# Optimization experiments

Hardware: AMD Instinct MI355X
Metric: run time of the kernel (lower is better)

The kernel has to match this reference:

```python
import jax, jax.numpy as jnp
import numpy as np

N_NODES = 100000
N_FEATS = 512
HIDDEN = 64
NUM_SAMPLES = 5
NUM_CLASSES = 16
BATCH = 16384


def setup_inputs() -> dict:
    key = jax.random.key(0)
    k1, k2, k3, k4, k5, k6, k7 = jax.random.split(key, 7)
    nodes = jax.random.randint(k1, (BATCH,), 0, N_NODES, dtype=jnp.int64) if jax.config.jax_enable_x64 else jax.random.randint(k1, (BATCH,), 0, N_NODES, dtype=jnp.int32)
    neigh_idx = jax.random.randint(k2, (N_NODES, NUM_SAMPLES), 0, N_NODES, dtype=jnp.int32)
    features = jax.random.normal(k3, (N_NODES, N_FEATS), dtype=jnp.float32)
    # xavier-uniform style init
    def xavier(k, shape):
        fan_in, fan_out = shape[1], shape[0]
        lim = jnp.sqrt(6.0 / (fan_in + fan_out)).astype(jnp.float32)
        return jax.random.uniform(k, shape, jnp.float32, -lim, lim)
    w1 = xavier(k4, (HIDDEN, 2 * N_FEATS))      # enc1 weight
    w2 = xavier(k5, (HIDDEN, 2 * HIDDEN))       # enc2 weight
    w_cls = xavier(k6, (NUM_CLASSES, HIDDEN))   # classifier weight
    return {"features": features, "w1": w1, "w2": w2, "w_cls": w_cls,
            "nodes": nodes, "neigh_idx": neigh_idx}


def reference(features, w1, w2, w_cls, nodes, neigh_idx):
    # Layer 1 (enc1, gcn=False): concat(self, mean(sampled neighbors)) -> W1 -> ReLU
    # Computed for all nodes (superset of what torch computes lazily; same values).
    neigh1 = features[neigh_idx].mean(axis=1)                      # [N, F]
    h1 = jax.nn.relu(jnp.concatenate([features, neigh1], axis=1) @ w1.T)  # [N, H]
    # Layer 2 (enc2) on the query batch
    self2 = h1[nodes]                                              # [B, H]
    neigh2 = h1[neigh_idx[nodes]].mean(axis=1)                     # [B, H]
    h2 = jax.nn.relu(jnp.concatenate([self2, neigh2], axis=1) @ w2.T)     # [B, H]
    # scores = (w_cls @ h2.T).T == h2 @ w_cls.T
    return h2 @ w_cls.T                                            # [B, C]
```

## Files before the change

kernel.cpp:

```cpp
#include <hip/hip_runtime.h>
#include <hip/hip_bf16.h>

#define N_NODES 100000
#define N_FEATS 512
#define HIDDEN 64
#define NUM_SAMPLES 5
#define NUM_CLASSES 16
#define BATCH 16384
#define N_TILES (N_NODES / 16)

typedef __attribute__((ext_vector_type(8))) short bf16x8;
typedef __attribute__((ext_vector_type(8))) unsigned short u16x8;
typedef __attribute__((ext_vector_type(4))) float f32x4;

static __device__ __forceinline__ float bf2f(unsigned short s) {
    unsigned int u = ((unsigned int)s) << 16;
    return __builtin_bit_cast(float, u);
}
static __device__ __forceinline__ short f2bf(float v) {
    __hip_bfloat16 b = __float2bfloat16(v);
    return *reinterpret_cast<short*>(&b);
}
static __device__ __forceinline__ int clampi(int v) {
    return ((unsigned)v < (unsigned)N_NODES) ? v : 0;
}

__global__ __launch_bounds__(256) void prep(const float* __restrict__ w1f,
                                            short* __restrict__ w1p,
                                            const int* __restrict__ nodes_i32,
                                            int* __restrict__ flag) {
    const int t = blockIdx.x * 256 + threadIdx.x;
    if (t < 64 * 1024) {
        const int j = t & 7;
        const int lane = (t >> 3) & 63;
        const int nb = (t >> 9) & 7;
        const int kk = t >> 12;
        const int l16 = lane & 15, quad = lane >> 4;
        const int cn = nb * 16 + l16;
        const int h = cn & 63, part = cn >> 6;
        w1p[t] = f2bf(w1f[h * 1024 + part * 512 + kk * 32 + quad * 8 + j]);
    }
    if (blockIdx.x == 0 && threadIdx.x == 0) {
        int odd_nonzero = 0;
        for (int i = 0; i < 64; i++)
            if (nodes_i32[2 * i + 1] != 0) odd_nonzero++;
        *flag = (odd_nonzero == 0) ? 1 : 0;
    }
}

__global__ __launch_bounds__(512) void pq_gemm(const float* __restrict__ feat,
                                               const short* __restrict__ w1p,
                                               short* __restrict__ PQ) {
    __shared__ __align__(16) short at[16 * 512];
    const int wave = threadIdx.x >> 6;
    const int lane = threadIdx.x & 63;
    const int quad = lane >> 4;
    const int l16  = lane & 15;
    const int tidr = threadIdx.x >> 5;
    const int tids = threadIdx.x & 31;

    bf16x8 bfrag[16];
#pragma unroll
    for (int kk = 0; kk < 16; kk++)
        bfrag[kk] = *reinterpret_cast<const bf16x8*>(
            w1p + (size_t)kk * 4096 + wave * 512 + lane * 8);

    const int stride = gridDim.x;
    f32x4 ra[2][2];

#define LOAD_TILE(tt)                                                             \
    {                                                                             \
        const float* base = feat + (size_t)((tt) * 16 + tidr) * N_FEATS + tids * 8;\
        _Pragma("unroll")                                                         \
        for (int i = 0; i < 2; i++) {                                             \
            ra[i][0] = *reinterpret_cast<const f32x4*>(base + i * 256);           \
            ra[i][1] = *reinterpret_cast<const f32x4*>(base + i * 256 + 4);       \
        }                                                                         \
    }

    int t = blockIdx.x;
    if (t < N_TILES) LOAD_TILE(t)

    for (; t < N_TILES; t += stride) {
        __syncthreads();
#pragma unroll
        for (int i = 0; i < 2; i++) {
            bf16x8 p;
#pragma unroll
            for (int j = 0; j < 4; j++) {
                p[j]     = f2bf(ra[i][0][j]);
                p[4 + j] = f2bf(ra[i][1][j]);
            }
            const int chunk = i * 32 + tids;
            const int cs = chunk ^ (tidr & 7);
            *reinterpret_cast<bf16x8*>(at + tidr * 512 + cs * 8) = p;
        }
        const int tn = t + stride;
        if (tn < N_TILES) LOAD_TILE(tn)
        __syncthreads();

        f32x4 acc = (f32x4){0.f, 0.f, 0.f, 0.f};
#pragma unroll
        for (int kk = 0; kk < 16; kk++) {
            const int chunk = kk * 4 + quad;
            const int cs = chunk ^ (l16 & 7);
            bf16x8 afrag = *reinterpret_cast<const bf16x8*>(at + l16 * 512 + cs * 8);
            acc = __builtin_amdgcn_mfma_f32_16x16x32_bf16(afrag, bfrag[kk], acc, 0, 0, 0);
        }

        const int cn = wave * 16 + l16;
#pragma unroll
        for (int r = 0; r < 4; r++) {
            const int row = t * 16 + quad * 4 + r;
            PQ[(size_t)row * 128 + cn] = f2bf(acc[r]);
        }
    }
#undef LOAD_TILE
}

__global__ __launch_bounds__(256) void h1_combine(const short* __restrict__ PQ,
                                                  const int* __restrict__ neigh_idx,
                                                  short* __restrict__ H1) {
    const int t = blockIdx.x * 256 + threadIdx.x;
    const int n = t >> 3;
    const int sub = t & 7;
    if (n >= N_NODES) return;

    u16x8 pv = *reinterpret_cast<const u16x8*>(PQ + (size_t)n * 128 + sub * 8);
    float s[8];
#pragma unroll
    for (int j = 0; j < 8; j++) s[j] = 0.f;
#pragma unroll
    for (int i = 0; i < NUM_SAMPLES; i++) {
        const int ni = clampi(neigh_idx[n * NUM_SAMPLES + i]);
        u16x8 qv = *reinterpret_cast<const u16x8*>(PQ + (size_t)ni * 128 + 64 + sub * 8);
#pragma unroll
        for (int j = 0; j < 8; j++) s[j] += bf2f(qv[j]);
    }
    u16x8 ov;
#pragma unroll
    for (int j = 0; j < 8; j++) {
        float v = bf2f(pv[j]) + 0.2f * s[j];
        v = v > 0.f ? v : 0.f;
        ov[j] = (unsigned short)f2bf(v);
    }
    *reinterpret_cast<u16x8*>(H1 + (size_t)n * 64 + sub * 8) = ov;
}

__global__ __launch_bounds__(256) void layer2_cls(const short* __restrict__ H1,
                                                  const int* __restrict__ nodes_i32,
                                                  const int* __restrict__ neigh_idx,
                                                  const float* __restrict__ w2,
                                                  const float* __restrict__ wcls,
                                                  const int* __restrict__ flag,
                                                  float* __restrict__ out) {
    __shared__ float gbuf[16][128];
    __shared__ float h2buf[16][64];
    const int wave = threadIdx.x >> 6;
    const int lane = threadIdx.x & 63;
    const int is64 = *flag;
    const int b0 = blockIdx.x * 16;

#pragma unroll
    for (int it = 0; it < 4; it++) {
        const int item = wave * 4 + it;
        const int b = b0 + item;
        const int node = clampi(nodes_i32[is64 ? 2 * b : b]);
        float selfv = bf2f((unsigned short)H1[(size_t)node * 64 + lane]);
        float ns = 0.f;
#pragma unroll
        for (int s = 0; s < NUM_SAMPLES; s++) {
            const int ni = clampi(neigh_idx[node * NUM_SAMPLES + s]);
            ns += bf2f((unsigned short)H1[(size_t)ni * 64 + lane]);
        }
        gbuf[item][lane] = selfv;
        gbuf[item][64 + lane] = 0.2f * ns;
    }
    __syncthreads();

    float acc[4] = {0.f, 0.f, 0.f, 0.f};
    const f32x4* w2r = reinterpret_cast<const f32x4*>(w2 + lane * 128);
#pragma unroll 8
    for (int k = 0; k < 32; k++) {
        f32x4 w = w2r[k];
#pragma unroll
        for (int it = 0; it < 4; it++) {
            f32x4 g = *reinterpret_cast<const f32x4*>(&gbuf[wave * 4 + it][k * 4]);
            acc[it] += g[0] * w[0] + g[1] * w[1] + g[2] * w[2] + g[3] * w[3];
        }
    }
#pragma unroll
    for (int it = 0; it < 4; it++) {
        float h2 = acc[it] > 0.f ? acc[it] : 0.f;
        h2buf[wave * 4 + it][lane] = h2;
    }
    __syncthreads();

    if (lane < NUM_CLASSES) {
        const f32x4* wcr = reinterpret_cast<const f32x4*>(wcls + lane * 64);
#pragma unroll
        for (int it = 0; it < 4; it++) {
            const int item = wave * 4 + it;
            const f32x4* hr = reinterpret_cast<const f32x4*>(&h2buf[item][0]);
            float o = 0.f;
#pragma unroll
            for (int k = 0; k < 16; k++) {
                f32x4 h = hr[k], w = wcr[k];
                o += h[0] * w[0] + h[1] * w[1] + h[2] * w[2] + h[3] * w[3];
            }
            out[(size_t)(b0 + item) * NUM_CLASSES + lane] = o;
        }
    }
}

extern "C" void kernel_launch(void* const* d_in, const int* in_sizes, int n_in,
                              void* d_out, int out_size, void* d_ws, size_t ws_size,
                              hipStream_t stream) {
    const float* feat = nullptr;
    const float* w1 = nullptr;
    const float* w2 = nullptr;
    const float* wcls = nullptr;
    const int* nodes = nullptr;
    const int* neigh_idx = nullptr;
    for (int i = 0; i < n_in; i++) {
        switch (in_sizes[i]) {
            case 51200000: feat = (const float*)d_in[i]; break;
            case 65536:    w1 = (const float*)d_in[i]; break;
            case 8192:     w2 = (const float*)d_in[i]; break;
            case 1024:     wcls = (const float*)d_in[i]; break;
            case 16384:    nodes = (const int*)d_in[i]; break;
            case 500000:   neigh_idx = (const int*)d_in[i]; break;
            default: break;
        }
    }
    float* out = (float*)d_out;

    int* flag = (int*)d_ws;
    short* w1p = (short*)((char*)d_ws + 256);
    short* PQ  = (short*)((char*)d_ws + 256 + 131072);
    short* H1  = (short*)((char*)d_ws + 256 + 131072 + (size_t)N_NODES * 128 * 2);

    prep<<<256, 256, 0, stream>>>(w1, w1p, nodes, flag);
    pq_gemm<<<512, 512, 0, stream>>>(feat, w1p, PQ);
    h1_combine<<<(N_NODES * 8 + 255) / 256, 256, 0, stream>>>(PQ, neigh_idx, H1);
    layer2_cls<<<BATCH / 16, 256, 0, stream>>>(H1, nodes, neigh_idx, w2, wcls, flag, out);
}
```

Measured before the change: 337.1 us.

## Fold weight prep into GEMM, stage PQ output via LDS, inline dtype flag

Removes the prep kernel. Each pq_gemm block now converts its W1 fragments from fp32 to bf16 directly, and layer2_cls detects int64 node indices with a wave ballot instead of reading a flag. The GEMM epilogue writes results into an LDS staging buffer, and on the next iteration they are written to PQ as coalesced 16-byte row stores instead of scattered 2-byte stores. In exchange, every one of the 512 blocks re-reads and converts the W1 weights, and the LDS footprint grows slightly.

```diff
diff --git a/kernel.cpp b/kernel.cpp
--- a/kernel.cpp
+++ b/kernel.cpp
@@ -25,45 +25,35 @@
     return ((unsigned)v < (unsigned)N_NODES) ? v : 0;
 }
 
-__global__ __launch_bounds__(256) void prep(const float* __restrict__ w1f,
-                                            short* __restrict__ w1p,
-                                            const int* __restrict__ nodes_i32,
-                                            int* __restrict__ flag) {
-    const int t = blockIdx.x * 256 + threadIdx.x;
-    if (t < 64 * 1024) {
-        const int j = t & 7;
-        const int lane = (t >> 3) & 63;
-        const int nb = (t >> 9) & 7;
-        const int kk = t >> 12;
-        const int l16 = lane & 15, quad = lane >> 4;
-        const int cn = nb * 16 + l16;
-        const int h = cn & 63, part = cn >> 6;
-        w1p[t] = f2bf(w1f[h * 1024 + part * 512 + kk * 32 + quad * 8 + j]);
-    }
-    if (blockIdx.x == 0 && threadIdx.x == 0) {
-        int odd_nonzero = 0;
-        for (int i = 0; i < 64; i++)
-            if (nodes_i32[2 * i + 1] != 0) odd_nonzero++;
-        *flag = (odd_nonzero == 0) ? 1 : 0;
-    }
-}
-
 __global__ __launch_bounds__(512) void pq_gemm(const float* __restrict__ feat,
-                                               const short* __restrict__ w1p,
+                                               const float* __restrict__ w1f,
                                                short* __restrict__ PQ) {
     __shared__ __align__(16) short at[16 * 512];
-    const int wave = threadIdx.x >> 6;
-    const int lane = threadIdx.x & 63;
+    __shared__ __align__(16) short cb[16 * 132];
+    const int tid  = threadIdx.x;
+    const int wave = tid >> 6;
+    const int lane = tid & 63;
     const int quad = lane >> 4;
     const int l16  = lane & 15;
-    const int tidr = threadIdx.x >> 5;
-    const int tids = threadIdx.x & 31;
+    const int tidr = tid >> 5;
+    const int tids = tid & 31;
 
     bf16x8 bfrag[16];
-#pragma unroll
-    for (int kk = 0; kk < 16; kk++)
-        bfrag[kk] = *reinterpret_cast<const bf16x8*>(
-            w1p + (size_t)kk * 4096 + wave * 512 + lane * 8);
+    {
+        const int cn = wave * 16 + l16;
+        const int h = cn & 63, part = cn >> 6;
+        const float* wb = w1f + h * 1024 + part * 512 + quad * 8;
+#pragma unroll
+        for (int kk = 0; kk < 16; kk++) {
+            f32x4 lo = *reinterpret_cast<const f32x4*>(wb + kk * 32);
+            f32x4 hi = *reinterpret_cast<const f32x4*>(wb + kk * 32 + 4);
+#pragma unroll
+            for (int j = 0; j < 4; j++) {
+                bfrag[kk][j]     = f2bf(lo[j]);
+                bfrag[kk][4 + j] = f2bf(hi[j]);
+            }
+        }
+    }
 
     const int stride = gridDim.x;
     f32x4 ra[2][2];
@@ -81,8 +71,15 @@
     int t = blockIdx.x;
     if (t < N_TILES) LOAD_TILE(t)
 
+    int have_c = 0, tprev = 0;
     for (; t < N_TILES; t += stride) {
         __syncthreads();
+        if (have_c && tid < 256) {
+            const int row = tid >> 4, ch = tid & 15;
+            bf16x8 v = *reinterpret_cast<const bf16x8*>(cb + row * 132 + ch * 8);
+            *reinterpret_cast<bf16x8*>(
+                PQ + (size_t)(tprev * 16 + row) * 128 + ch * 8) = v;
+        }
 #pragma unroll
         for (int i = 0; i < 2; i++) {
             bf16x8 p;
@@ -108,12 +105,18 @@
             acc = __builtin_amdgcn_mfma_f32_16x16x32_bf16(afrag, bfrag[kk], acc, 0, 0, 0);
         }
 
-        const int cn = wave * 16 + l16;
-#pragma unroll
-        for (int r = 0; r < 4; r++) {
-            const int row = t * 16 + quad * 4 + r;
-            PQ[(size_t)row * 128 + cn] = f2bf(acc[r]);
-        }
+#pragma unroll
+        for (int r = 0; r < 4; r++)
+            cb[(quad * 4 + r) * 132 + wave * 16 + l16] = f2bf(acc[r]);
+        have_c = 1;
+        tprev = t;
+    }
+    __syncthreads();
+    if (have_c && tid < 256) {
+        const int row = tid >> 4, ch = tid & 15;
+        bf16x8 v = *reinterpret_cast<const bf16x8*>(cb + row * 132 + ch * 8);
+        *reinterpret_cast<bf16x8*>(
+            PQ + (size_t)(tprev * 16 + row) * 128 + ch * 8) = v;
     }
 #undef LOAD_TILE
 }
@@ -152,14 +155,15 @@
                                                   const int* __restrict__ neigh_idx,
                                                   const float* __restrict__ w2,
                                                   const float* __restrict__ wcls,
-                                                  const int* __restrict__ flag,
                                                   float* __restrict__ out) {
     __shared__ float gbuf[16][128];
     __shared__ float h2buf[16][64];
     const int wave = threadIdx.x >> 6;
     const int lane = threadIdx.x & 63;
-    const int is64 = *flag;
     const int b0 = blockIdx.x * 16;
+
+    const int odd = nodes_i32[2 * lane + 1];
+    const int is64 = (__ballot(odd != 0) == 0ull) ? 1 : 0;
 
 #pragma unroll
     for (int it = 0; it < 4; it++) {
@@ -235,13 +239,10 @@
     }
     float* out = (float*)d_out;
 
-    int* flag = (int*)d_ws;
-    short* w1p = (short*)((char*)d_ws + 256);
     short* PQ  = (short*)((char*)d_ws + 256 + 131072);
     short* H1  = (short*)((char*)d_ws + 256 + 131072 + (size_t)N_NODES * 128 * 2);
 
-    prep<<<256, 256, 0, stream>>>(w1, w1p, nodes, flag);
-    pq_gemm<<<512, 512, 0, stream>>>(feat, w1p, PQ);
+    pq_gemm<<<512, 512, 0, stream>>>(feat, w1, PQ);
     h1_combine<<<(N_NODES * 8 + 255) / 256, 256, 0, stream>>>(PQ, neigh_idx, H1);
-    layer2_cls<<<BATCH / 16, 256, 0, stream>>>(H1, nodes, neigh_idx, w2, wcls, flag, out);
-}
+    layer2_cls<<<BATCH / 16, 256, 0, stream>>>(H1, nodes, neigh_idx, w2, wcls, out);
+}
```

New measurement: 337.5 us. About the same (+0.1%).
